# Performance work log

Measured on AMD Instinct MI355X. Metric: run time of the kernel, lower is better.

## Reference

```python
import jax, jax.numpy as jnp
import numpy as np

NH, NP = 8, 16          # num_head, num_att_points
MIN_A, MAX_A = 0.25, 0.75
BN_EPS = 1e-5


def conv1x1(x, W, b=None):
    # x: (B,C,H,W), W: (O,C) -> (B,O,H,W)
    y = jnp.einsum('bchw,oc->bohw', x, W)
    return y if b is None else y + b[None, :, None, None]


def setup_inputs() -> dict:
    key = jax.random.key(0)
    ks = jax.random.split(key, 12)
    B, C, H, W_ = 2, 256, 64, 64
    s = 1.0 / np.sqrt(C)
    return {
        'feat_sd': jax.random.normal(ks[0], (B, C, H, W_), jnp.float32),
        'value_proj_w': jax.random.normal(ks[1], (C, C), jnp.float32) * s,
        'value_proj_b': jax.random.normal(ks[2], (C,), jnp.float32) * 0.01,
        'size_deform_w': jax.random.normal(ks[3], (2 * NH, C), jnp.float32) * s,
        'size_deform_b': jax.random.normal(ks[4], (2 * NH,), jnp.float32) * 0.01,
        'anchor_deform_w': jax.random.normal(ks[5], (NH * NP * 2, C), jnp.float32) * s,
        'anchor_deform_b': jax.random.normal(ks[6], (NH * NP * 2,), jnp.float32) * 0.01,
        'anchor_att_w': jax.random.normal(ks[7], (NH * NP, C), jnp.float32) * s,
        'anchor_att_b': jax.random.normal(ks[8], (NH * NP,), jnp.float32) * 0.01,
        'out_proj_w': jax.random.normal(ks[9], (C, C), jnp.float32) * s,
        'bn_gamma': jax.random.uniform(ks[10], (C,), jnp.float32, 0.5, 1.5),
        'bn_beta': jax.random.normal(ks[11], (C,), jnp.float32) * 0.01,
    }


def _forward(feat_sd, value_proj_w, value_proj_b, size_deform_w, size_deform_b,
             anchor_deform_w, anchor_deform_b, anchor_att_w, anchor_att_b,
             out_proj_w, bn_gamma, bn_beta):
    B, C, H, W_ = feat_sd.shape
    L = H * W_
    hd = C // NH
    eps = 1e-6

    memory = conv1x1(feat_sd, value_proj_w, value_proj_b)  # value pool (B,C,H,W)

    # ----- reference windows: normalized pixel centers + learned per-head box sizes -----
    yc = (jnp.arange(1, H + 1, dtype=feat_sd.dtype) - 0.5) / (H + eps)
    xc = (jnp.arange(1, W_ + 1, dtype=feat_sd.dtype) - 0.5) / (W_ + eps)
    cy, cx = jnp.meshgrid(yc, xc, indexing='ij')
    center = jnp.stack([cx, cy], axis=-1).reshape(L, 2)  # (L,2), [x,y]

    size = jnp.clip(jax.nn.sigmoid(conv1x1(feat_sd, size_deform_w, size_deform_b)), MIN_A, MAX_A)
    size = size.reshape(B, 2 * NH, L).transpose(0, 2, 1).reshape(B, L, NH, 2)

    # ----- learned sampling offsets within each reference window -----
    offset = jax.nn.sigmoid(conv1x1(feat_sd, anchor_deform_w, anchor_deform_b))
    offset = offset.reshape(B, NH * NP * 2, L).transpose(0, 2, 1).reshape(B, L, NH, NP, 2)

    size_e = size[:, :, :, None, :]
    grid = jnp.clip(center[None, :, None, None, :] - 0.5 * size_e + offset * size_e, 0.0, 1.0)
    grid = grid.transpose(0, 2, 1, 3, 4)  # (B,NH,L,NP,2)

    # ----- bilinear grid_sample (align_corners=True; grid in [0,1] so no padding hit) -----
    ix = grid[..., 0] * (W_ - 1)
    iy = grid[..., 1] * (H - 1)
    x0 = jnp.floor(ix)
    y0 = jnp.floor(iy)
    wx = ix - x0
    wy = iy - y0
    x0i = jnp.clip(x0.astype(jnp.int32), 0, W_ - 1)
    x1i = jnp.clip(x0i + 1, 0, W_ - 1)
    y0i = jnp.clip(y0.astype(jnp.int32), 0, H - 1)
    y1i = jnp.clip(y0i + 1, 0, H - 1)

    vflat = memory.reshape(B, NH, hd, H * W_)

    def gather(yi, xi):
        idx = (yi * W_ + xi).reshape(B, NH, 1, L * NP)
        g = jnp.take_along_axis(vflat, jnp.broadcast_to(idx, (B, NH, hd, L * NP)), axis=3)
        return g.reshape(B, NH, hd, L, NP)

    w00 = ((1 - wx) * (1 - wy))[:, :, None, :, :]
    w01 = (wx * (1 - wy))[:, :, None, :, :]
    w10 = ((1 - wx) * wy)[:, :, None, :, :]
    w11 = (wx * wy)[:, :, None, :, :]
    sampled_v = (gather(y0i, x0i) * w00 + gather(y0i, x1i) * w01 +
                 gather(y1i, x0i) * w10 + gather(y1i, x1i) * w11)  # (B,NH,hd,L,NP)

    # ----- static attention weights over sample points -----
    attn = conv1x1(feat_sd, anchor_att_w, anchor_att_b)              # (B,NH*NP,H,W)
    attn = attn.reshape(B, NH, NP, L).transpose(0, 1, 3, 2)          # (B,NH,L,NP)
    attn = jax.nn.softmax(attn, axis=-1)[:, :, None, :, :]           # (B,NH,1,L,NP)

    out = (attn * sampled_v).sum(-1).reshape(B, C, H, W_)            # heads-major == torch view

    # ----- out_proj: 1x1 conv (no bias) + BatchNorm2d (eval: mean=0, var=1) -----
    out = conv1x1(out, out_proj_w)
    scale = bn_gamma / jnp.sqrt(1.0 + BN_EPS)
    return out * scale[None, :, None, None] + bn_beta[None, :, None, None]


def reference(feat_sd, value_proj_w, value_proj_b, size_deform_w, size_deform_b,
              anchor_deform_w, anchor_deform_b, anchor_att_w, anchor_att_b,
              out_proj_w, bn_gamma, bn_beta):
    return _forward(feat_sd, value_proj_w, value_proj_b, size_deform_w, size_deform_b,
                    anchor_deform_w, anchor_deform_b, anchor_att_w, anchor_att_b,
                    out_proj_w, bn_gamma, bn_beta)
```

## Files before the change

kernel.cpp:

```cpp
#include <hip/hip_runtime.h>
#include <math.h>

#define LL 4096
#define KK 256
#define HH 64
#define WW 64
#define NHEAD 8
#define NPNT 16
#define HD 32
#define AST 264

typedef unsigned short u16;
typedef __attribute__((ext_vector_type(4))) float f32x4;
typedef __attribute__((ext_vector_type(2))) _Float16 h2;
typedef __attribute__((ext_vector_type(8))) _Float16 h8;

__device__ __forceinline__ u16 f2h(float x) {
    _Float16 h = (_Float16)x;
    return __builtin_bit_cast(unsigned short, h);
}

__global__ __launch_bounds__(256) void wprep_k(
    const float* __restrict__ vw,  const float* __restrict__ vb,
    const float* __restrict__ adw, const float* __restrict__ adb,
    const float* __restrict__ atw, const float* __restrict__ atb,
    const float* __restrict__ sw,  const float* __restrict__ sb,
    const float* __restrict__ pw,
    u16* __restrict__ wh,
    float* __restrict__ bcat,
    u16* __restrict__ ph)
{
    const int row = blockIdx.x * 4 + (threadIdx.x >> 6);
    const int c   = threadIdx.x & 63;

    if (row < 768) {
        const float* src = nullptr;
        float bv = 0.f;
        const int o = row;
        if (o < 256)      { src = vw  + (size_t)o * KK;        bv = vb[o]; }
        else if (o < 512) { src = adw + (size_t)(o-256) * KK;  bv = adb[o-256]; }
        else if (o < 640) { src = atw + (size_t)(o-512) * KK;  bv = atb[o-512]; }
        else if (o < 656) { src = sw  + (size_t)(o-640) * KK;  bv = sb[o-640]; }
        if (c == 0) bcat[o] = bv;

        float4 v = {0.f, 0.f, 0.f, 0.f};
        if (src) v = *(const float4*)(src + c * 4);
        ushort4 hv;
        hv.x = f2h(v.x); hv.y = f2h(v.y); hv.z = f2h(v.z); hv.w = f2h(v.w);
        *(ushort4*)(wh + (size_t)row * KK + c * 4) = hv;
    } else {
        const int o = row - 768;
        float4 v = *(const float4*)(pw + (size_t)o * KK + c * 4);
        ushort4 hv;
        hv.x = f2h(v.x); hv.y = f2h(v.y); hv.z = f2h(v.z); hv.w = f2h(v.w);
        *(ushort4*)(ph + (size_t)o * KK + c * 4) = hv;
    }
}

__global__ __launch_bounds__(512, 4) void projf_k(
    const float* __restrict__ feat,
    const u16* __restrict__ Wh,
    const float* __restrict__ bias,
    u16* __restrict__ mem2, float* __restrict__ rawp)
{
    __shared__ u16 Ah[64][AST];

    const int bx = blockIdx.x;
    const int gy = bx % 3;
    const int mb = bx / 3;
    const int m0g = mb * 64;
    const int b   = m0g >> 12;
    const int l0  = m0g & (LL - 1);
    const int tid = threadIdx.x;
    const bool VAL = (gy == 0);

    {
        const int px = tid & 63;
        const int kb = (tid >> 6) * 32;
        const float* fp = feat + ((size_t)(b * KK + kb)) * LL + l0 + px;
        #pragma unroll
        for (int cch = 0; cch < 4; ++cch) {
            float xs[8];
            #pragma unroll
            for (int j = 0; j < 8; ++j)
                xs[j] = fp[(size_t)(cch * 8 + j) * LL];
            ushort4 a, c;
            a.x = f2h(xs[0]); a.y = f2h(xs[1]); a.z = f2h(xs[2]); a.w = f2h(xs[3]);
            c.x = f2h(xs[4]); c.y = f2h(xs[5]); c.z = f2h(xs[6]); c.w = f2h(xs[7]);
            *(ushort4*)&Ah[px][kb + cch * 8]     = a;
            *(ushort4*)&Ah[px][kb + cch * 8 + 4] = c;
        }
    }
    __syncthreads();

    const int lam  = tid & 63;
    const int wave = tid >> 6;

    if (gy == 2 && wave >= 5) return;

    const int row  = lam & 15;
    const int kq   = (lam >> 4) * 8;
    const int n0   = gy * 256 + wave * 32;

    f32x4 acc[4][2];
    #pragma unroll
    for (int i = 0; i < 4; ++i)
        #pragma unroll
        for (int j = 0; j < 2; ++j)
            acc[i][j] = (f32x4){0.f, 0.f, 0.f, 0.f};

    #pragma unroll
    for (int s = 0; s < 8; ++s) {
        const int k0 = s * 32;
        h8 ah[4], bh[2];
        #pragma unroll
        for (int mf = 0; mf < 4; ++mf)
            ah[mf] = *(const h8*)(const void*)&Ah[mf * 16 + row][k0 + kq];
        #pragma unroll
        for (int nf = 0; nf < 2; ++nf)
            bh[nf] = *(const h8*)(const void*)(Wh + ((size_t)(n0 + nf * 16 + row)) * KK + k0 + kq);
        #pragma unroll
        for (int mf = 0; mf < 4; ++mf)
            #pragma unroll
            for (int nf = 0; nf < 2; ++nf)
                acc[mf][nf] = __builtin_amdgcn_mfma_f32_16x16x32_f16(ah[mf], bh[nf], acc[mf][nf], 0, 0, 0);
    }

    float bj[2];
    #pragma unroll
    for (int nf = 0; nf < 2; ++nf) bj[nf] = bias[n0 + nf * 16 + row];

    #pragma unroll
    for (int mf = 0; mf < 4; ++mf)
        #pragma unroll
        for (int r = 0; r < 4; ++r) {
            const int m  = m0g + mf * 16 + 4 * (lam >> 4) + r;
            const int bb = m >> 12;
            const int ll = m & (LL - 1);
            #pragma unroll
            for (int nf = 0; nf < 2; ++nf) {
                const int o = n0 + nf * 16 + row;
                const float v = acc[mf][nf][r] + bj[nf];
                if (VAL) {
                    mem2[(((size_t)(bb * NHEAD + (o >> 5)) * LL + ll) * HD) + (o & 31)] = f2h(v);
                } else if (o < 640) {
                    rawp[((size_t)(bb * LL + ll)) * 400 + (o - 240)] = v;
                } else if (o < 656) {
                    rawp[((size_t)(bb * LL + ll)) * 400 + (o - 640)] = v;
                }
            }
        }
}

__global__ __launch_bounds__(64) void mgemm1_k(
    const u16* __restrict__ Ah,
    const u16* __restrict__ Bh,
    const float* __restrict__ gamma, const float* __restrict__ beta,
    float* __restrict__ out)
{
    const int lam = threadIdx.x;
    const int m0 = blockIdx.x * 64;
    const int n0 = blockIdx.y * 64;
    const int row = lam & 15;
    const int kq  = (lam >> 4) * 8;

    f32x4 acc[4][4];
    #pragma unroll
    for (int i = 0; i < 4; ++i)
        #pragma unroll
        for (int j = 0; j < 4; ++j)
            acc[i][j] = (f32x4){0.f, 0.f, 0.f, 0.f};

    #pragma unroll
    for (int s = 0; s < 8; ++s) {
        const int k0 = s * 32;
        h8 ah[4], bh[4];
        #pragma unroll
        for (int mf = 0; mf < 4; ++mf)
            ah[mf] = *(const h8*)(const void*)(Ah + ((size_t)(m0 + mf * 16 + row)) * KK + k0 + kq);
        #pragma unroll
        for (int nf = 0; nf < 4; ++nf)
            bh[nf] = *(const h8*)(const void*)(Bh + ((size_t)(n0 + nf * 16 + row)) * KK + k0 + kq);
        #pragma unroll
        for (int mf = 0; mf < 4; ++mf)
            #pragma unroll
            for (int nf = 0; nf < 4; ++nf)
                acc[mf][nf] = __builtin_amdgcn_mfma_f32_16x16x32_f16(ah[mf], bh[nf], acc[mf][nf], 0, 0, 0);
    }

    #pragma unroll
    for (int mf = 0; mf < 4; ++mf)
        #pragma unroll
        for (int r = 0; r < 4; ++r) {
            const int o = m0 + mf * 16 + 4 * (lam >> 4) + r;
            const float sc = gamma[o] / sqrtf(1.f + 1e-5f);
            const float be = beta[o];
            #pragma unroll
            for (int nf = 0; nf < 4; ++nf) {
                const int lg = n0 + nf * 16 + row;
                const int b  = lg >> 12;
                const int ll = lg & (LL - 1);
                out[((size_t)(b * KK + o)) * LL + ll] = acc[mf][nf][r] * sc + be;
            }
        }
}

__global__ __launch_bounds__(256) void sample5_k(
    const u16* __restrict__ mem2,
    const float* __restrict__ rawp,
    u16* __restrict__ preH)
{
    __shared__ float srec[32][17][4];

    const int tid = threadIdx.x;

    #pragma unroll
    for (int q = 0; q < 2; ++q) {
        const int t  = q * 256 + tid;
        const int gi = t >> 4;
        const int p  = t & 15;
        const int g  = blockIdx.x * 32 + gi;
        const int l  = g & (LL - 1);
        const int h  = (g >> 12) & (NHEAD - 1);
        const int b  = g >> 15;
        const float* rb = rawp + ((size_t)(b * LL + l)) * 400;

        float logit = rb[272 + h * NPNT + p];
        float m = logit;
        m = fmaxf(m, __shfl_xor(m, 1));
        m = fmaxf(m, __shfl_xor(m, 2));
        m = fmaxf(m, __shfl_xor(m, 4));
        m = fmaxf(m, __shfl_xor(m, 8));
        float e = __expf(logit - m);
        float s = e;
        s += __shfl_xor(s, 1);
        s += __shfl_xor(s, 2);
        s += __shfl_xor(s, 4);
        s += __shfl_xor(s, 8);
        const float wp = e / s;

        float s0 = rb[h * 2 + 0];
        float s1 = rb[h * 2 + 1];
        s0 = fminf(fmaxf(1.f / (1.f + __expf(-s0)), 0.25f), 0.75f);
        s1 = fminf(fmaxf(1.f / (1.f + __expf(-s1)), 0.25f), 0.75f);

        const float2 oo = *(const float2*)(rb + 16 + (h * NPNT + p) * 2);
        const float o0 = 1.f / (1.f + __expf(-oo.x));
        const float o1 = 1.f / (1.f + __expf(-oo.y));

        const int xl = l & (WW - 1);
        const int yl = l >> 6;
        const float cx = ((float)xl + 0.5f) / ((float)WW + 1e-6f);
        const float cy = ((float)yl + 0.5f) / ((float)HH + 1e-6f);

        float gx = fminf(fmaxf(cx - 0.5f * s0 + o0 * s0, 0.f), 1.f);
        float gy = fminf(fmaxf(cy - 0.5f * s1 + o1 * s1, 0.f), 1.f);
        const float ix = gx * (float)(WW - 1);
        const float iy = gy * (float)(HH - 1);
        const int x0 = min(max((int)floorf(ix), 0), WW - 2);
        const int y0 = min(max((int)floorf(iy), 0), HH - 2);
        const float wx = ix - (float)x0;
        const float wy = iy - (float)y0;

        srec[gi][p][0] = __int_as_float((y0 * WW + x0) * HD);
        srec[gi][p][1] = wx;
        srec[gi][p][2] = wy;
        srec[gi][p][3] = wp;
    }
    __syncthreads();

    const int gi = tid >> 3;
    const int j  = tid & 7;
    const int g  = blockIdx.x * 32 + gi;
    const int l  = g & (LL - 1);
    const int h  = (g >> 12) & (NHEAD - 1);
    const int b  = g >> 15;
    const u16* mb = mem2 + (size_t)(b * NHEAD + h) * LL * HD + j * 8;
    const bool hiSide = (j >= 4);

    float acc[8] = {};
    #pragma unroll
    for (int p = 0; p < NPNT; ++p) {
        const float4 rec = *(const float4*)&srec[gi][p][0];
        const int off   = __float_as_int(rec.x);
        const float fx  = hiSide ? rec.y : (1.f - rec.y);
        const float wf  = rec.w * fx;
        const h2 wp2 = __builtin_bit_cast(h2,
            __builtin_amdgcn_cvt_pkrtz(wf * (1.f - rec.z), wf * rec.z));
        const u16* p0 = mb + off;
        const uint4 V0 = *(const uint4*)(const void*)p0;
        const uint4 V1 = *(const uint4*)(const void*)(p0 + WW * HD);
        const unsigned v0w[4] = {V0.x, V0.y, V0.z, V0.w};
        const unsigned v1w[4] = {V1.x, V1.y, V1.z, V1.w};
        #pragma unroll
        for (int wd = 0; wd < 4; ++wd) {
            const unsigned plo = __builtin_amdgcn_perm(v1w[wd], v0w[wd], 0x05040100u);
            const unsigned phi = __builtin_amdgcn_perm(v1w[wd], v0w[wd], 0x07060302u);
            acc[2*wd]   = __builtin_amdgcn_fdot2(__builtin_bit_cast(h2, plo), wp2, acc[2*wd],   false);
            acc[2*wd+1] = __builtin_amdgcn_fdot2(__builtin_bit_cast(h2, phi), wp2, acc[2*wd+1], false);
        }
    }

    #pragma unroll
    for (int e = 0; e < 8; ++e)
        acc[e] += __shfl_xor(acc[e], 4);

    if (j < 4) {
        ushort4 ha, hb;
        ha.x = f2h(acc[0]); ha.y = f2h(acc[1]); ha.z = f2h(acc[2]); ha.w = f2h(acc[3]);
        hb.x = f2h(acc[4]); hb.y = f2h(acc[5]); hb.z = f2h(acc[6]); hb.w = f2h(acc[7]);
        u16* dst = preH + ((size_t)(b * LL + l)) * KK + h * HD + j * 8;
        *(ushort4*)dst       = ha;
        *(ushort4*)(dst + 4) = hb;
    }
}

extern "C" void kernel_launch(void* const* d_in, const int* in_sizes, int n_in,
                              void* d_out, int out_size, void* d_ws, size_t ws_size,
                              hipStream_t stream) {
    const float* feat  = (const float*)d_in[0];
    const float* vw    = (const float*)d_in[1];
    const float* vb    = (const float*)d_in[2];
    const float* sw    = (const float*)d_in[3];
    const float* sb    = (const float*)d_in[4];
    const float* adw   = (const float*)d_in[5];
    const float* adb   = (const float*)d_in[6];
    const float* atw   = (const float*)d_in[7];
    const float* atb   = (const float*)d_in[8];
    const float* pw    = (const float*)d_in[9];
    const float* gamma = (const float*)d_in[10];
    const float* beta  = (const float*)d_in[11];
    float* out = (float*)d_out;
    char* ws = (char*)d_ws;

    u16* mem2   = (u16*)(ws + 0);
    float* rawp = (float*)(ws + 4194304);
    u16* preH   = (u16*)(ws + 17301504);
    u16* wch    = (u16*)(ws + 21495808);
    float* bcat = (float*)(ws + 21889024);
    u16* pwh    = (u16*)(ws + 21892096);

    wprep_k<<<dim3(256), dim3(256), 0, stream>>>(vw, vb, adw, adb, atw, atb,
                                                 sw, sb, pw, wch, bcat, pwh);
    projf_k<<<dim3(384), dim3(512), 0, stream>>>(feat, wch, bcat, mem2, rawp);
    sample5_k<<<dim3(2048), dim3(256), 0, stream>>>(mem2, rawp, preH);
    mgemm1_k<<<dim3(4, 128), dim3(64), 0, stream>>>(pwh, preH, gamma, beta, out);
}
```

Measured before the change: 50.84 us.

## Store projection logits in fp16 and retile projection GEMM to 32-row blocks

The intermediate buffer of offset, size and attention logits (rawp) is now stored as fp16 instead of fp32, halving its write and read traffic between the projection and sampling kernels. The projection GEMM is retiled from 64-row blocks with 512 threads to 32-row blocks with 256 threads, each wave computing 32x64 outputs, which doubles the block count to 768. Workspace offsets are compacted to match. Rounding logits and offsets to fp16 adds error to the sampling positions and softmax weights.

```diff
diff --git a/kernel.cpp b/kernel.cpp
--- a/kernel.cpp
+++ b/kernel.cpp
@@ -18,6 +18,9 @@
 __device__ __forceinline__ u16 f2h(float x) {
     _Float16 h = (_Float16)x;
     return __builtin_bit_cast(unsigned short, h);
+}
+__device__ __forceinline__ float h2f(u16 h) {
+    return (float)__builtin_bit_cast(_Float16, h);
 }
 
 __global__ __launch_bounds__(256) void wprep_k(
@@ -57,26 +60,26 @@
     }
 }
 
-__global__ __launch_bounds__(512, 4) void projf_k(
+__global__ __launch_bounds__(256) void projf_k(
     const float* __restrict__ feat,
     const u16* __restrict__ Wh,
     const float* __restrict__ bias,
-    u16* __restrict__ mem2, float* __restrict__ rawp)
+    u16* __restrict__ mem2, u16* __restrict__ rawp)
 {
-    __shared__ u16 Ah[64][AST];
+    __shared__ u16 Ah[32][AST];
 
     const int bx = blockIdx.x;
     const int gy = bx % 3;
     const int mb = bx / 3;
-    const int m0g = mb * 64;
+    const int m0g = mb * 32;
     const int b   = m0g >> 12;
     const int l0  = m0g & (LL - 1);
     const int tid = threadIdx.x;
     const bool VAL = (gy == 0);
 
     {
-        const int px = tid & 63;
-        const int kb = (tid >> 6) * 32;
+        const int px = tid & 31;
+        const int kb = (tid >> 5) * 32;
         const float* fp = feat + ((size_t)(b * KK + kb)) * LL + l0 + px;
         #pragma unroll
         for (int cch = 0; cch < 4; ++cch) {
@@ -96,57 +99,57 @@
     const int lam  = tid & 63;
     const int wave = tid >> 6;
 
-    if (gy == 2 && wave >= 5) return;
+    if (gy == 2 && wave == 3) return;
 
     const int row  = lam & 15;
     const int kq   = (lam >> 4) * 8;
-    const int n0   = gy * 256 + wave * 32;
-
-    f32x4 acc[4][2];
-    #pragma unroll
-    for (int i = 0; i < 4; ++i)
-        #pragma unroll
-        for (int j = 0; j < 2; ++j)
+    const int n0   = gy * 256 + wave * 64;
+
+    f32x4 acc[2][4];
+    #pragma unroll
+    for (int i = 0; i < 2; ++i)
+        #pragma unroll
+        for (int j = 0; j < 4; ++j)
             acc[i][j] = (f32x4){0.f, 0.f, 0.f, 0.f};
 
     #pragma unroll
     for (int s = 0; s < 8; ++s) {
         const int k0 = s * 32;
-        h8 ah[4], bh[2];
-        #pragma unroll
-        for (int mf = 0; mf < 4; ++mf)
+        h8 ah[2], bh[4];
+        #pragma unroll
+        for (int mf = 0; mf < 2; ++mf)
             ah[mf] = *(const h8*)(const void*)&Ah[mf * 16 + row][k0 + kq];
         #pragma unroll
-        for (int nf = 0; nf < 2; ++nf)
+        for (int nf = 0; nf < 4; ++nf)
             bh[nf] = *(const h8*)(const void*)(Wh + ((size_t)(n0 + nf * 16 + row)) * KK + k0 + kq);
         #pragma unroll
-        for (int mf = 0; mf < 4; ++mf)
-            #pragma unroll
-            for (int nf = 0; nf < 2; ++nf)
+        for (int mf = 0; mf < 2; ++mf)
+            #pragma unroll
+            for (int nf = 0; nf < 4; ++nf)
                 acc[mf][nf] = __builtin_amdgcn_mfma_f32_16x16x32_f16(ah[mf], bh[nf], acc[mf][nf], 0, 0, 0);
     }
 
-    float bj[2];
-    #pragma unroll
-    for (int nf = 0; nf < 2; ++nf) bj[nf] = bias[n0 + nf * 16 + row];
-
-    #pragma unroll
-    for (int mf = 0; mf < 4; ++mf)
+    float bj[4];
+    #pragma unroll
+    for (int nf = 0; nf < 4; ++nf) bj[nf] = bias[n0 + nf * 16 + row];
+
+    #pragma unroll
+    for (int mf = 0; mf < 2; ++mf)
         #pragma unroll
         for (int r = 0; r < 4; ++r) {
             const int m  = m0g + mf * 16 + 4 * (lam >> 4) + r;
             const int bb = m >> 12;
             const int ll = m & (LL - 1);
             #pragma unroll
-            for (int nf = 0; nf < 2; ++nf) {
+            for (int nf = 0; nf < 4; ++nf) {
                 const int o = n0 + nf * 16 + row;
                 const float v = acc[mf][nf][r] + bj[nf];
                 if (VAL) {
                     mem2[(((size_t)(bb * NHEAD + (o >> 5)) * LL + ll) * HD) + (o & 31)] = f2h(v);
                 } else if (o < 640) {
-                    rawp[((size_t)(bb * LL + ll)) * 400 + (o - 240)] = v;
+                    rawp[((size_t)(bb * LL + ll)) * 400 + (o - 240)] = f2h(v);
                 } else if (o < 656) {
-                    rawp[((size_t)(bb * LL + ll)) * 400 + (o - 640)] = v;
+                    rawp[((size_t)(bb * LL + ll)) * 400 + (o - 640)] = f2h(v);
                 }
             }
         }
@@ -207,7 +210,7 @@
 
 __global__ __launch_bounds__(256) void sample5_k(
     const u16* __restrict__ mem2,
-    const float* __restrict__ rawp,
+    const u16* __restrict__ rawp,
     u16* __restrict__ preH)
 {
     __shared__ float srec[32][17][4];
@@ -223,9 +226,9 @@
         const int l  = g & (LL - 1);
         const int h  = (g >> 12) & (NHEAD - 1);
         const int b  = g >> 15;
-        const float* rb = rawp + ((size_t)(b * LL + l)) * 400;
-
-        float logit = rb[272 + h * NPNT + p];
+        const u16* rb = rawp + ((size_t)(b * LL + l)) * 400;
+
+        float logit = h2f(rb[272 + h * NPNT + p]);
         float m = logit;
         m = fmaxf(m, __shfl_xor(m, 1));
         m = fmaxf(m, __shfl_xor(m, 2));
@@ -239,14 +242,14 @@
         s += __shfl_xor(s, 8);
         const float wp = e / s;
 
-        float s0 = rb[h * 2 + 0];
-        float s1 = rb[h * 2 + 1];
+        float s0 = h2f(rb[h * 2 + 0]);
+        float s1 = h2f(rb[h * 2 + 1]);
         s0 = fminf(fmaxf(1.f / (1.f + __expf(-s0)), 0.25f), 0.75f);
         s1 = fminf(fmaxf(1.f / (1.f + __expf(-s1)), 0.25f), 0.75f);
 
-        const float2 oo = *(const float2*)(rb + 16 + (h * NPNT + p) * 2);
-        const float o0 = 1.f / (1.f + __expf(-oo.x));
-        const float o1 = 1.f / (1.f + __expf(-oo.y));
+        const unsigned oo = *(const unsigned*)(const void*)(rb + 16 + (h * NPNT + p) * 2);
+        const float o0 = 1.f / (1.f + __expf(-h2f((u16)(oo & 0xffffu))));
+        const float o1 = 1.f / (1.f + __expf(-h2f((u16)(oo >> 16))));
 
         const int xl = l & (WW - 1);
         const int yl = l >> 6;
@@ -334,15 +337,15 @@
     char* ws = (char*)d_ws;
 
     u16* mem2   = (u16*)(ws + 0);
-    float* rawp = (float*)(ws + 4194304);
-    u16* preH   = (u16*)(ws + 17301504);
-    u16* wch    = (u16*)(ws + 21495808);
-    float* bcat = (float*)(ws + 21889024);
-    u16* pwh    = (u16*)(ws + 21892096);
+    u16* rawp   = (u16*)(ws + 4194304);
+    u16* preH   = (u16*)(ws + 10747904);
+    u16* wch    = (u16*)(ws + 14942208);
+    float* bcat = (float*)(ws + 15335424);
+    u16* pwh    = (u16*)(ws + 15339520);
 
     wprep_k<<<dim3(256), dim3(256), 0, stream>>>(vw, vb, adw, adb, atw, atb,
                                                  sw, sb, pw, wch, bcat, pwh);
-    projf_k<<<dim3(384), dim3(512), 0, stream>>>(feat, wch, bcat, mem2, rawp);
+    projf_k<<<dim3(768), dim3(256), 0, stream>>>(feat, wch, bcat, mem2, rawp);
     sample5_k<<<dim3(2048), dim3(256), 0, stream>>>(mem2, rawp, preH);
     mgemm1_k<<<dim3(4, 128), dim3(64), 0, stream>>>(pwh, preH, gamma, beta, out);
 }
```

New measurement: 52.42 us. +3.1%, slower.
